# Optimization experiments

Hardware: AMD Instinct MI355X
Metric: run time of the kernel (lower is better)

The kernel has to match this reference:

```python
import jax, jax.numpy as jnp
import numpy as np

N, D_IN, D_OUT = 65536, 1024, 256


def setup_inputs() -> dict:
    key = jax.random.key(0)
    k_x, k_wm, k_bm, k_ws, k_bs = jax.random.split(key, 5)
    x = jax.random.normal(k_x, (N, D_IN), dtype=jnp.float32)
    # nn.Linear params (stored transposed for x @ W convenience)
    W_mu = jax.random.normal(k_wm, (D_IN, D_OUT), dtype=jnp.float32) * 0.02
    b_mu = jax.random.normal(k_bm, (D_OUT,), dtype=jnp.float32) * 0.02
    W_log_std = jax.random.normal(k_ws, (D_IN, D_OUT), dtype=jnp.float32) * 0.02
    b_log_std = jax.random.normal(k_bs, (D_OUT,), dtype=jnp.float32) * 0.02
    return {"x": x, "W_mu": W_mu, "b_mu": b_mu,
            "W_log_std": W_log_std, "b_log_std": b_log_std}


def reference(x, W_mu, b_mu, W_log_std, b_log_std):
    # mean and log_std heads
    mean = x @ W_mu + b_mu                      # [n, j]
    log_std = x @ W_log_std + b_log_std         # [n, j]
    variance = jnp.exp(2.0 * log_std)           # exp(2*log_std)
    # Original builds diag covariance eye(j)*var and Cholesky-samples via
    # MultivariateNormal.rsample; for a diagonal covariance this is exactly
    # z = mean + sqrt(variance) * eps.
    eps = jax.random.normal(jax.random.key(42), mean.shape, dtype=mean.dtype)
    z = mean + jnp.sqrt(variance) * eps
    return (mean, variance, z)
```

## Files before the change

kernel.cpp:

```cpp
#include <hip/hip_runtime.h>
#include <stdint.h>

#define N_ROWS 65536
#define K_DIM  1024
#define J_OUT  256
#define ROWS_PB 64
#define NT64 16
#define THREADS 512

typedef _Float16 half8 __attribute__((ext_vector_type(8)));
typedef _Float16 half4 __attribute__((ext_vector_type(4)));
typedef float    f32x4 __attribute__((ext_vector_type(4)));

__device__ __forceinline__ uint32_t rotl32(uint32_t v, uint32_t r) {
  return __builtin_amdgcn_alignbit(v, v, 32u - r);
}
__device__ __forceinline__ uint32_t tf_bits_xor(uint32_t ctr) {
  const uint32_t ks0 = 0u, ks1 = 42u, ks2 = 0x1BD11BF0u;
  uint32_t x0 = 0u;
  uint32_t x1 = ctr + ks1;
#define TF_R(rr) x0 += x1; x1 = rotl32(x1, rr) ^ x0;
  TF_R(13) TF_R(15) TF_R(26) TF_R(6)
  x0 += ks1; x1 += ks2 + 1u;
  TF_R(17) TF_R(29) TF_R(16) TF_R(24)
  x0 += ks2; x1 += ks0 + 2u;
  TF_R(13) TF_R(15) TF_R(26) TF_R(6)
  x0 += ks0; x1 += ks1 + 3u;
  TF_R(17) TF_R(29) TF_R(16) TF_R(24)
  x0 += ks1; x1 += ks2 + 4u;
  TF_R(13) TF_R(15) TF_R(26) TF_R(6)
  x0 += ks2; x1 += ks0 + 5u;
#undef TF_R
  return x0 ^ x1;
}

__device__ __forceinline__ float eps_from_bits(uint32_t bits) {
  float f = __uint_as_float((bits >> 9) | 0x3F800000u) - 1.0f;
  float u = fmaxf(-0.99999994f, f * 2.0f - 0.99999994f);
  float w = __builtin_amdgcn_logf((1.0f - u) * (1.0f + u)) * (-0.6931471805599453f);
  float t = w - 2.5f;
  float p = 2.81022636e-08f;
  p = fmaf(p, t, 3.43273939e-07f);
  p = fmaf(p, t, -3.5233877e-06f);
  p = fmaf(p, t, -4.39150654e-06f);
  p = fmaf(p, t, 0.00021858087f);
  p = fmaf(p, t, -0.00125372503f);
  p = fmaf(p, t, -0.00417768164f);
  p = fmaf(p, t, 0.246640727f);
  p = fmaf(p, t, 1.50140941f);
  if (w >= 5.0f) {
    float s = sqrtf(w) - 3.0f;
    float q = -0.000200214257f;
    q = fmaf(q, s, 0.000100950558f);
    q = fmaf(q, s, 0.00134934322f);
    q = fmaf(q, s, -0.00367342844f);
    q = fmaf(q, s, 0.00573950773f);
    q = fmaf(q, s, -0.0076224613f);
    q = fmaf(q, s, -0.00943887047f);
    q = fmaf(q, s, 1.00167406f);
    q = fmaf(q, s, 2.83297682f);
    p = q;
  }
  return 1.41421354f * (p * u);
}

__global__ void pack_w_kernel(const float* __restrict__ Wmu,
                              const float* __restrict__ Wls,
                              _Float16* __restrict__ wt) {
  const int chunk = blockIdx.x * blockDim.x + threadIdx.x;
  const int lane = chunk & 63;
  const int n  = (chunk >> 6) & 3;
  const int ks = (chunk >> 8) & 1;
  const int w  = (chunk >> 9) & 7;
  const int t  = chunk >> 12;
  const int k0 = t * 64 + ks * 32 + (lane >> 4) * 8;
  const int c  = w * 32 + (n >> 1) * 16 + (lane & 15);
  const float* W = (n & 1) ? Wls : Wmu;
  half8 v;
#pragma unroll
  for (int e = 0; e < 8; ++e) v[e] = (_Float16)W[(size_t)(k0 + e) * J_OUT + c];
  *(half8*)(wt + (size_t)chunk * 8) = v;
}

#define KBARRIER() asm volatile("s_waitcnt lgkmcnt(0)\n\ts_barrier" ::: "memory")

#define KSTEP(T, BC, BN, SA0, SA1)                                             \
  {                                                                            \
    const _Float16* Ar_ = Abuf + ((T) & 1) * (ROWS_PB * 80);                   \
    _Float16* Aw_ = Abuf + (((T) + 1) & 1) * (ROWS_PB * 80);                   \
    if ((T) + 1 < NT64) {                                                      \
      half4 h0_, h1_;                                                          \
      _Pragma("unroll") for (int e = 0; e < 4; ++e) {                          \
        h0_[e] = (_Float16)SA0[e]; h1_[e] = (_Float16)SA1[e];                  \
      }                                                                        \
      *(half4*)(Aw_ + swaddr) = h0_;                                           \
      *(half4*)(Aw_ + swaddr + 32 * 80) = h1_;                                 \
    }                                                                          \
    if ((T) + 3 < NT64) {                                                      \
      SA0 = *(const f32x4*)(sp0 + ((T) + 3) * 64);                             \
      SA1 = *(const f32x4*)(sp1 + ((T) + 3) * 64);                             \
    }                                                                          \
    if ((T) + 1 < NT64) {                                                      \
      const _Float16* bbn_ = bbase + (size_t)((T) + 1) * 32768;                \
      _Pragma("unroll") for (int i = 0; i < 8; ++i)                            \
        BN[i] = *(const half8*)(bbn_ + i * 512);                               \
    }                                                                          \
    _Pragma("unroll") for (int ks = 0; ks < 2; ++ks) {                         \
      half8 af_[4];                                                            \
      _Pragma("unroll") for (int m = 0; m < 4; ++m)                            \
        af_[m] = *(const half8*)(Ar_ + arbase + m * 1280 + ks * 32);           \
      _Pragma("unroll") for (int m = 0; m < 4; ++m)                            \
        _Pragma("unroll") for (int n = 0; n < 4; ++n)                          \
          acc[m][n] = __builtin_amdgcn_mfma_f32_16x16x32_f16(                  \
              af_[m], BC[ks * 4 + n], acc[m][n], 0, 0, 0);                     \
    }                                                                          \
    KBARRIER();                                                                \
  }

__global__ __launch_bounds__(THREADS, 4)
void fused_heads_kernel(const float* __restrict__ x,
                        const _Float16* __restrict__ wt,
                        const float* __restrict__ b_mu,
                        const float* __restrict__ b_ls,
                        float* __restrict__ out) {
  __shared__ __align__(16) unsigned char smem[ROWS_PB * 80 * 2 * 2 > 16 * 260 * 4
                                              ? ROWS_PB * 80 * 2 * 2 : 16 * 260 * 4];
  _Float16* Abuf = (_Float16*)smem;
  float*    ebuf = (float*)smem;

  const int tid  = threadIdx.x;
  const int lane = tid & 63;
  const int w    = tid >> 6;
  const int rowbase = blockIdx.x * ROWS_PB;

  const int srow = tid >> 4, skc = tid & 15;
  const float* sp0 = x + (size_t)(rowbase + srow) * K_DIM + skc * 4;
  const float* sp1 = sp0 + (size_t)32 * K_DIM;
  const int swaddr = srow * 80 + skc * 4;

  const int arbase = (lane & 15) * 80 + (lane >> 4) * 8;
  const _Float16* bbase = wt + ((size_t)w << 12) + lane * 8;

  f32x4 acc[4][4] = {};

  {
    const f32x4 s0 = *(const f32x4*)(sp0);
    const f32x4 s1 = *(const f32x4*)(sp1);
    half4 h0, h1;
#pragma unroll
    for (int e = 0; e < 4; ++e) { h0[e] = (_Float16)s0[e]; h1[e] = (_Float16)s1[e]; }
    *(half4*)(&Abuf[swaddr]) = h0;
    *(half4*)(&Abuf[swaddr + 32 * 80]) = h1;
  }
  f32x4 sAa0 = *(const f32x4*)(sp0 + 64),  sAa1 = *(const f32x4*)(sp1 + 64);
  f32x4 sAb0 = *(const f32x4*)(sp0 + 128), sAb1 = *(const f32x4*)(sp1 + 128);
  half8 bfA[8], bfB[8];
#pragma unroll
  for (int i = 0; i < 8; ++i) bfA[i] = *(const half8*)(bbase + i * 512);
  KBARRIER();

#pragma unroll
  for (int tt = 0; tt < 8; ++tt) {
    KSTEP(2 * tt,     bfA, bfB, sAa0, sAa1)
    KSTEP(2 * tt + 1, bfB, bfA, sAb0, sAb1)
  }

  float* out_mean = out;
  float* out_var  = out + (size_t)N_ROWS * J_OUT;
  float* out_z    = out + 2 * (size_t)N_ROWS * J_OUT;
  const int colq = lane & 15;
  const int g4   = (lane >> 4) * 4;

#pragma unroll
  for (int q = 0; q < 2; ++q) {
    const int c = w * 32 + q * 16 + colq;
    const float bm = b_mu[c];
    const float bl = b_ls[c];
#pragma unroll
    for (int m = 0; m < 4; ++m)
#pragma unroll
      for (int e = 0; e < 4; ++e) {
        acc[m][2 * q][e]     = acc[m][2 * q][e] + bm;
        acc[m][2 * q + 1][e] = __expf(2.0f * (acc[m][2 * q + 1][e] + bl));
      }
  }

#pragma unroll
  for (int m = 0; m < 4; ++m)
#pragma unroll
    for (int arr = 0; arr < 3; ++arr) {
#pragma unroll
      for (int q = 0; q < 2; ++q) {
        const int lcol = w * 32 + q * 16 + colq;
#pragma unroll
        for (int e = 0; e < 4; ++e) {
          const int lrow = g4 + e;
          float val;
          if (arr == 0) {
            val = acc[m][2 * q][e];
          } else if (arr == 1) {
            val = acc[m][2 * q + 1][e];
          } else {
            const uint32_t ctr =
                (uint32_t)((rowbase + m * 16 + lrow) * J_OUT + lcol);
            val = fmaf(sqrtf(acc[m][2 * q + 1][e]),
                       eps_from_bits(tf_bits_xor(ctr)), acc[m][2 * q][e]);
          }
          ebuf[lrow * 260 + lcol] = val;
        }
      }
      KBARRIER();
      float* oarr = (arr == 0) ? out_mean : (arr == 1) ? out_var : out_z;
#pragma unroll
      for (int i = 0; i < 2; ++i) {
        const int idx = i * THREADS + tid;
        const int r  = idx >> 6;
        const int c4 = idx & 63;
        const f32x4 v = *(const f32x4*)(ebuf + r * 260 + c4 * 4);
        *(f32x4*)(oarr + (size_t)(rowbase + m * 16 + r) * J_OUT + c4 * 4) = v;
      }
      KBARRIER();
    }
}

extern "C" void kernel_launch(void* const* d_in, const int* in_sizes, int n_in,
                              void* d_out, int out_size, void* d_ws, size_t ws_size,
                              hipStream_t stream) {
  const float* x   = (const float*)d_in[0];
  const float* Wmu = (const float*)d_in[1];
  const float* bmu = (const float*)d_in[2];
  const float* Wls = (const float*)d_in[3];
  const float* bls = (const float*)d_in[4];
  float* out = (float*)d_out;
  _Float16* wt = (_Float16*)d_ws;

  pack_w_kernel<<<256, 256, 0, stream>>>(Wmu, Wls, wt);
  fused_heads_kernel<<<N_ROWS / ROWS_PB, THREADS, 0, stream>>>(x, wt, bmu, bls, out);
}
```

Baseline: 163.1 us.

## Write epilogue outputs directly from registers instead of staging through LDS

The epilogue no longer stages each output array through a shared-memory tile with barriers before coalesced float4 stores. Each lane now writes mean, variance and z straight from its MFMA accumulators using scalar stores, removing 24 barriers and the LDS round trips. It also computes the std as exp(log_std) and the variance as its square, which avoids a sqrt. The cost is scalar 4-byte stores: each row's 16 contiguous columns form 64-byte segments spread across rows, which may coalesce worse on this write-heavy output.

```diff
diff --git a/kernel.cpp b/kernel.cpp
--- a/kernel.cpp
+++ b/kernel.cpp
@@ -123,11 +123,7 @@
                         const float* __restrict__ b_mu,
                         const float* __restrict__ b_ls,
                         float* __restrict__ out) {
-  __shared__ __align__(16) unsigned char smem[ROWS_PB * 80 * 2 * 2 > 16 * 260 * 4
-                                              ? ROWS_PB * 80 * 2 * 2 : 16 * 260 * 4];
-  _Float16* Abuf = (_Float16*)smem;
-  float*    ebuf = (float*)smem;
-
+  __shared__ __align__(16) _Float16 Abuf[2 * ROWS_PB * 80];
   const int tid  = threadIdx.x;
   const int lane = tid & 63;
   const int w    = tid >> 6;
@@ -177,50 +173,22 @@
     const float bm = b_mu[c];
     const float bl = b_ls[c];
 #pragma unroll
-    for (int m = 0; m < 4; ++m)
+    for (int m = 0; m < 4; ++m) {
+      const int r0 = rowbase + m * 16 + g4;
 #pragma unroll
       for (int e = 0; e < 4; ++e) {
-        acc[m][2 * q][e]     = acc[m][2 * q][e] + bm;
-        acc[m][2 * q + 1][e] = __expf(2.0f * (acc[m][2 * q + 1][e] + bl));
+        const float mean = acc[m][2 * q][e] + bm;
+        const float s    = __expf(acc[m][2 * q + 1][e] + bl);
+        const float var  = s * s;
+        const uint32_t ctr = (uint32_t)((r0 + e) * J_OUT + c);
+        const float z = fmaf(s, eps_from_bits(tf_bits_xor(ctr)), mean);
+        const size_t off = (size_t)(r0 + e) * J_OUT + c;
+        out_mean[off] = mean;
+        out_var[off]  = var;
+        out_z[off]    = z;
       }
-  }
-
-#pragma unroll
-  for (int m = 0; m < 4; ++m)
-#pragma unroll
-    for (int arr = 0; arr < 3; ++arr) {
-#pragma unroll
-      for (int q = 0; q < 2; ++q) {
-        const int lcol = w * 32 + q * 16 + colq;
-#pragma unroll
-        for (int e = 0; e < 4; ++e) {
-          const int lrow = g4 + e;
-          float val;
-          if (arr == 0) {
-            val = acc[m][2 * q][e];
-          } else if (arr == 1) {
-            val = acc[m][2 * q + 1][e];
-          } else {
-            const uint32_t ctr =
-                (uint32_t)((rowbase + m * 16 + lrow) * J_OUT + lcol);
-            val = fmaf(sqrtf(acc[m][2 * q + 1][e]),
-                       eps_from_bits(tf_bits_xor(ctr)), acc[m][2 * q][e]);
-          }
-          ebuf[lrow * 260 + lcol] = val;
-        }
-      }
-      KBARRIER();
-      float* oarr = (arr == 0) ? out_mean : (arr == 1) ? out_var : out_z;
-#pragma unroll
-      for (int i = 0; i < 2; ++i) {
-        const int idx = i * THREADS + tid;
-        const int r  = idx >> 6;
-        const int c4 = idx & 63;
-        const f32x4 v = *(const f32x4*)(ebuf + r * 260 + c4 * 4);
-        *(f32x4*)(oarr + (size_t)(rowbase + m * 16 + r) * J_OUT + c4 * 4) = v;
-      }
-      KBARRIER();
     }
+  }
 }
 
 extern "C" void kernel_launch(void* const* d_in, const int* in_sizes, int n_in,
```

Measured after the change: 180.2 us. 1.11x slower.
